# Performance work log

Hardware: AMD Instinct MI355X
Metric: run time of the kernel (lower is better)

## Reference

```python
import jax, jax.numpy as jnp
import numpy as np

N, E, C, A, R = 10000, 128000, 128, 10, 8  # nodes, edges, channels, elements, radial basis


def setup_inputs() -> dict:
    key = jax.random.key(0)
    ks = jax.random.split(key, 16)
    inp = {
        'node_attrs': jax.random.uniform(ks[0], (N, A), dtype=jnp.float32),
        'node_feats': jax.random.normal(ks[1], (N, 4 * C), dtype=jnp.float32),
        'edge_attrs': jax.random.normal(ks[2], (E, 4), dtype=jnp.float32),
        'edge_feats': jax.random.normal(ks[3], (E, R), dtype=jnp.float32),
        'edge_index': jax.random.randint(ks[4], (2, E), 0, N, dtype=jnp.int32),
        # linear_up (per-l channel mixing 128->128)
        'W_up0': jax.random.normal(ks[5], (C, C), dtype=jnp.float32),
        'W_up1': jax.random.normal(ks[6], (C, C), dtype=jnp.float32),
        # radial MLP hs=[8,64,64,64,512]
        'R0': jax.random.normal(ks[7], (R, 64), dtype=jnp.float32),
        'R1': jax.random.normal(ks[8], (64, 64), dtype=jnp.float32),
        'R2': jax.random.normal(ks[9], (64, 64), dtype=jnp.float32),
        'R3': jax.random.normal(ks[10], (64, 4 * C), dtype=jnp.float32),
        # density net hs=[8,1]
        'W_density': jax.random.normal(ks[11], (R, 1), dtype=jnp.float32),
        # linear: irreps_mid (256x0e+256x1o) -> target (128x0e+128x1o)
        'W_lin0': jax.random.normal(ks[12], (2 * C, C), dtype=jnp.float32),
        'W_lin1': jax.random.normal(ks[13], (2 * C, C), dtype=jnp.float32),
        # skip_tp: FullyConnectedTP(node_feats, node_attrs(scalars)) -> hidden
        'W_skip0': jax.random.normal(ks[14], (C, A, C), dtype=jnp.float32),
        'W_skip1': jax.random.normal(ks[15], (C, A, C), dtype=jnp.float32),
    }
    return inp


def reference(node_attrs, node_feats, edge_attrs, edge_feats, edge_index,
              W_up0, W_up1, R0, R1, R2, R3, W_density, W_lin0, W_lin1,
              W_skip0, W_skip1):
    n = node_feats.shape[0]
    silu = jax.nn.silu
    x0 = node_feats[:, :C]                       # [N,128]  l=0
    x1 = node_feats[:, C:].reshape(n, C, 3)      # [N,128,3] l=1

    # skip_tp (node_attrs are scalars -> per-element channel mixing)
    norm_skip = 1.0 / np.sqrt(C * A)
    sc0 = jnp.einsum('nu,na,uav->nv', x0, node_attrs, W_skip0) * norm_skip
    sc1 = jnp.einsum('nuk,na,uav->nvk', x1, node_attrs, W_skip1) * norm_skip
    sc = jnp.concatenate([sc0, sc1.reshape(n, 3 * C)], axis=1)  # [N,512]

    # linear_up
    h0 = (x0 @ W_up0) / np.sqrt(C)
    h1 = jnp.einsum('nuk,uv->nvk', x1, W_up1) / np.sqrt(C)

    # radial MLP -> per-edge TP weights [E, 4*C]
    w = silu((edge_feats @ R0) / np.sqrt(R))
    w = silu((w @ R1) / np.sqrt(64))
    w = silu((w @ R2) / np.sqrt(64))
    w = (w @ R3) / np.sqrt(64)
    w1, w2, w3, w4 = jnp.split(w, 4, axis=1)     # each [E,128]

    # edge density
    edge_density = jnp.tanh(((edge_feats @ W_density) / np.sqrt(R)) ** 2)  # [E,1]

    sender = edge_index[0]
    receiver = edge_index[1]
    density = jax.ops.segment_sum(edge_density, receiver, num_segments=n)  # [N,1]

    # gather sender features
    hs0 = h0[sender]   # [E,128]
    hs1 = h1[sender]   # [E,128,3]
    y0 = edge_attrs[:, :1]   # [E,1]
    y1 = edge_attrs[:, 1:4]  # [E,3]

    # uvu tensor product paths (edge_irreps x edge_attrs -> irreps_mid)
    m0a = w1 * hs0 * y0                                      # 0e x 0e -> 0e
    m0b = w4 * jnp.einsum('euk,ek->eu', hs1, y1) / np.sqrt(3.0)  # 1o x 1o -> 0e
    m1a = (w2 * hs0)[:, :, None] * y1[:, None, :]            # 0e x 1o -> 1o
    m1b = w3[:, :, None] * hs1 * y0[:, :, None]              # 1o x 0e -> 1o

    mid0 = jnp.concatenate([m0a, m0b], axis=1)               # [E,256]
    mid1 = jnp.concatenate([m1a, m1b], axis=1)               # [E,256,3]

    # scatter messages to receivers
    M0 = jax.ops.segment_sum(mid0, receiver, num_segments=n)                     # [N,256]
    M1 = jax.ops.segment_sum(mid1.reshape(-1, 2 * C * 3), receiver, num_segments=n).reshape(n, 2 * C, 3)

    # linear irreps_mid -> target, then density normalization
    denom = density + 1.0
    out0 = (M0 @ W_lin0) / np.sqrt(2 * C) / denom                               # [N,128]
    out1 = jnp.einsum('nuk,uv->nvk', M1, W_lin1) / np.sqrt(2 * C) / denom[:, :, None]

    # reshape_irreps: [N, channels, sum(2l+1)] = [N,128,4]
    message = jnp.concatenate([out0[:, :, None], out1], axis=2)
    return message, sc
```

## Files before the change

### kernel.cpp

```cpp
#include <hip/hip_runtime.h>
#include <hip/hip_bf16.h>
#include <hip/hip_fp16.h>

#define N_NODES 10000
#define N_EDGES 128000
constexpr int C = 128;
constexpr int A = 10;

constexpr float INV_SQRT_C  = 0.08838834764831845f;
constexpr float INV_SQRT_R  = 0.35355339059327373f;
constexpr float INV_SQRT_64 = 0.125f;
constexpr float INV_SQRT_CA = 0.027950849718747374f;
constexpr float INV_SQRT_2C = 0.0625f;
constexpr float INV_SQRT_3  = 0.57735026918962576f;

typedef short short8 __attribute__((ext_vector_type(8)));
typedef _Float16 f16x8 __attribute__((ext_vector_type(8)));
typedef _Float16 f16x2 __attribute__((ext_vector_type(2)));
typedef float f32x4 __attribute__((ext_vector_type(4)));

__device__ __forceinline__ float silu_f(float x) { return x / (1.0f + __expf(-x)); }

__device__ __forceinline__ void atomic_add_f32(float* p, float v) {
  __hip_atomic_fetch_add(p, v, __ATOMIC_RELAXED, __HIP_MEMORY_SCOPE_AGENT);
}

__device__ __forceinline__ unsigned short f2h(float f) {
  return __builtin_bit_cast(unsigned short, (_Float16)f);
}

__device__ __forceinline__ unsigned int pk2h(float a, float b) {
  auto h = __builtin_amdgcn_cvt_pkrtz(a, b);
  return __builtin_bit_cast(unsigned int, h);
}

__device__ __forceinline__ unsigned int pkmul_h2(unsigned int x, unsigned int y) {
  const f16x2 a = __builtin_bit_cast(f16x2, x), b = __builtin_bit_cast(f16x2, y);
  return __builtin_bit_cast(unsigned int, a * b);
}

__device__ __forceinline__ float4 h4tof4(uint2 v) {
  const __half2 lo = __builtin_bit_cast(__half2, v.x);
  const __half2 hi = __builtin_bit_cast(__half2, v.y);
  const float2 flo = __half22float2(lo), fhi = __half22float2(hi);
  return make_float4(flo.x, flo.y, fhi.x, fhi.y);
}

__global__ __launch_bounds__(256) void k_node_up(
    const float* __restrict__ nf, const float* __restrict__ Wu0,
    const float* __restrict__ Wu1, __half* __restrict__ Hh) {
  __shared__ __align__(16) float xs[8][C][4];
  const int t = threadIdx.x;
  const int n0 = blockIdx.x * 8;
  for (int idx = t; idx < 8 * 512; idx += 256) {
    const int nn = idx >> 9, q = idx & 511;
    const float val = nf[(size_t)(n0 + nn) * 512 + q];
    if (q < C) xs[nn][q][0] = val;
    else { const int r = q - C; xs[nn][r / 3][1 + r % 3] = val; }
  }
  __syncthreads();
  const int g = t >> 7, v = t & 127;
  float acc[4][4] = {};
  for (int u = 0; u < C; ++u) {
    const float w0 = Wu0[u * C + v];
    const float w1 = Wu1[u * C + v];
#pragma unroll
    for (int nn = 0; nn < 4; ++nn) {
      const float4 xv = *(const float4*)&xs[g * 4 + nn][u][0];
      acc[nn][0] = fmaf(xv.x, w0, acc[nn][0]);
      acc[nn][1] = fmaf(xv.y, w1, acc[nn][1]);
      acc[nn][2] = fmaf(xv.z, w1, acc[nn][2]);
      acc[nn][3] = fmaf(xv.w, w1, acc[nn][3]);
    }
  }
#pragma unroll
  for (int nn = 0; nn < 4; ++nn) {
    const int n = n0 + g * 4 + nn;
    uint2 o;
    o.x = pk2h(acc[nn][0] * INV_SQRT_C, acc[nn][1] * INV_SQRT_C);
    o.y = pk2h(acc[nn][2] * INV_SQRT_C, acc[nn][3] * INV_SQRT_C);
    *(uint2*)&Hh[(size_t)n * 512 + v * 4] = o;
  }
}

__device__ __forceinline__ void cvtw(const float* __restrict__ src,
                                     unsigned short* __restrict__ dst,
                                     int idx, int lgN, int KT) {
  const int k = idx >> lgN;
  const int n = idx & ((1 << lgN) - 1);
  dst[((n * KT + (k >> 5)) << 5) + (k & 31)] = f2h(src[idx]);
}

__global__ __launch_bounds__(256) void k_prep(
    const float* __restrict__ W0, const float* __restrict__ W1,
    unsigned short* __restrict__ B0, unsigned short* __restrict__ B1,
    const float* __restrict__ R1, unsigned short* __restrict__ R1a,
    const float* __restrict__ R2, unsigned short* __restrict__ R2a,
    const float* __restrict__ R3, unsigned short* __restrict__ R3a,
    const int* __restrict__ eidx, int* __restrict__ counts) {
  const int b = blockIdx.x, t = threadIdx.x;
  if (b < 640) {
    const int idx = b * 256 + t;
    const int k = idx >> 7, col = idx & 127;
    const int u = k / 10, a = k - u * 10;
    const int kp = a * 128 + u;
    const int dst = ((kp >> 5) * 128 + col) * 32 + (kp & 31);
    B0[dst] = f2h(W0[idx]);
    B1[dst] = f2h(W1[idx]);
  } else if (b < 656) {
    cvtw(R1, R1a, (b - 640) * 256 + t, 6, 2);
  } else if (b < 672) {
    cvtw(R2, R2a, (b - 656) * 256 + t, 6, 2);
  } else if (b < 800) {
    cvtw(R3, R3a, (b - 672) * 256 + t, 9, 2);
  } else {
    const int e = (b - 800) * 256 + t;
    if (e < N_EDGES) atomicAdd(&counts[eidx[N_EDGES + e]], 1);
  }
}

__global__ __launch_bounds__(256) void k_skip_mfma(
    const float* __restrict__ nf, const float* __restrict__ attrs,
    const unsigned short* __restrict__ B0, const unsigned short* __restrict__ B1,
    float* __restrict__ out_sc) {
  __shared__ __align__(16) unsigned short xs[64][136];
  __shared__ float at[64][10];
  __shared__ __align__(16) unsigned short zs[2][64][40];

  const int t = threadIdx.x;
  const int wave = t >> 6, lane = t & 63;
  const bool isG0 = blockIdx.x < 157;
  const int r0 = isG0 ? blockIdx.x * 64 : (blockIdx.x - 157) * 64;
  const int rcount = isG0 ? 10000 : 30000;
  const unsigned short* __restrict__ Bsw = isG0 ? B0 : B1;

  for (int idx = t; idx < 64 * 128; idx += 256) {
    const int i = idx >> 7, u = idx & 127;
    const int r = r0 + i;
    float v = 0.f;
    if (r < rcount) {
      if (isG0) v = nf[(size_t)r * 512 + u];
      else {
        const int n = r / 3, kc = r - n * 3;
        v = nf[(size_t)n * 512 + 128 + u * 3 + kc];
      }
    }
    xs[i][u] = f2h(v);
  }
  for (int idx = t; idx < 640; idx += 256) {
    const int i = idx / 10, a = idx - (idx / 10) * 10;
    const int r = r0 + i;
    float v = 0.f;
    if (r < rcount) v = attrs[(size_t)(isG0 ? r : r / 3) * 10 + a];
    at[i][a] = v;
  }
  __syncthreads();

  const int m = lane & 15, q = lane >> 4;
  const int colB = wave * 32;
  const int rr = t >> 2;
  const int off = (t & 3) * 8;

  unsigned int atr2[10];
#pragma unroll
  for (int a = 0; a < 10; ++a) {
    const unsigned int h = f2h(at[rr][a]);
    atr2[a] = h | (h << 16);
  }

  f32x4 acc[4][2];
#pragma unroll
  for (int rt = 0; rt < 4; ++rt)
#pragma unroll
    for (int ct = 0; ct < 2; ++ct) acc[rt][ct] = (f32x4){0.f, 0.f, 0.f, 0.f};

#pragma unroll
  for (int a = 0; a < 10; ++a) {
    const unsigned int av2 = atr2[a];
#pragma unroll
    for (int kk = 0; kk < 4; ++kk) {
      const int kt = a * 4 + kk;
      const int buf = kt & 1;
      {
        const uint4 xv = *(const uint4*)&xs[rr][kk * 32 + off];
        uint4 z;
        z.x = pkmul_h2(xv.x, av2);
        z.y = pkmul_h2(xv.y, av2);
        z.z = pkmul_h2(xv.z, av2);
        z.w = pkmul_h2(xv.w, av2);
        *(uint4*)&zs[buf][rr][off] = z;
      }
      __syncthreads();

      f16x8 bfrag[2];
#pragma unroll
      for (int ct = 0; ct < 2; ++ct) {
        const unsigned short* bp =
            &Bsw[(size_t)(kt * 128 + colB + ct * 16 + m) * 32 + q * 8];
        bfrag[ct] = *(const f16x8*)bp;
      }
#pragma unroll
      for (int rt = 0; rt < 4; ++rt) {
        const f16x8 afrag = *(const f16x8*)&zs[buf][rt * 16 + m][q * 8];
#pragma unroll
        for (int ct = 0; ct < 2; ++ct)
          acc[rt][ct] = __builtin_amdgcn_mfma_f32_16x16x32_f16(
              afrag, bfrag[ct], acc[rt][ct], 0, 0, 0);
      }
    }
  }

#pragma unroll
  for (int rt = 0; rt < 4; ++rt) {
#pragma unroll
    for (int reg = 0; reg < 4; ++reg) {
      const int rloc = rt * 16 + q * 4 + reg;
      const int r = r0 + rloc;
      if (r < rcount) {
#pragma unroll
        for (int ct = 0; ct < 2; ++ct) {
          const int v = colB + ct * 16 + m;
          const float val = acc[rt][ct][reg] * INV_SQRT_CA;
          if (isG0) {
            out_sc[(size_t)r * 512 + v] = val;
          } else {
            const int n = r / 3, kc = r - (r / 3) * 3;
            out_sc[(size_t)n * 512 + 128 + v * 3 + kc] = val;
          }
        }
      }
    }
  }
}

__global__ __launch_bounds__(1024) void k_scan(const int* __restrict__ counts,
                                               int* __restrict__ offsets,
                                               int* __restrict__ cursor) {
  __shared__ int part[1024];
  const int t = threadIdx.x;
  int local[10];
  int s = 0;
#pragma unroll
  for (int i = 0; i < 10; ++i) {
    const int idx = t * 10 + i;
    const int c = (idx < N_NODES) ? counts[idx] : 0;
    local[i] = s;
    s += c;
  }
  part[t] = s;
  __syncthreads();
  for (int off = 1; off < 1024; off <<= 1) {
    const int add = (t >= off) ? part[t - off] : 0;
    __syncthreads();
    part[t] += add;
    __syncthreads();
  }
  const int pre = (t > 0) ? part[t - 1] : 0;
#pragma unroll
  for (int i = 0; i < 10; ++i) {
    const int idx = t * 10 + i;
    if (idx < N_NODES) {
      const int o = pre + local[i];
      offsets[idx] = o;
      cursor[idx] = o;
    }
  }
  if (t == 1023) offsets[N_NODES] = part[1023];
}

__global__ __launch_bounds__(256) void k_scatter(
    const int* __restrict__ eidx, const float* __restrict__ ea_g,
    const float* __restrict__ ef_g,
    int* __restrict__ cursor,
    int* __restrict__ snd_s, int* __restrict__ rcv_s,
    float* __restrict__ ea_s, float* __restrict__ ef_s) {
  const int e = blockIdx.x * 256 + threadIdx.x;
  if (e < N_EDGES) {
    const int r = eidx[N_EDGES + e];
    const int pos = atomicAdd(&cursor[r], 1);
    snd_s[pos] = eidx[e];
    rcv_s[pos] = r;
    ((float4*)ea_s)[pos] = ((const float4*)ea_g)[e];
    ((float4*)ef_s)[pos * 2]     = ((const float4*)ef_g)[e * 2];
    ((float4*)ef_s)[pos * 2 + 1] = ((const float4*)ef_g)[e * 2 + 1];
  }
}

__global__ __launch_bounds__(256, 4) void k_mlp_msg(
    const float* __restrict__ ef_s, const float* __restrict__ ea_s,
    const int* __restrict__ snd_s, const int* __restrict__ rcv_s,
    const int* __restrict__ offsets,
    const float* __restrict__ R0, const unsigned short* __restrict__ R1a,
    const unsigned short* __restrict__ R2a, const unsigned short* __restrict__ R3a,
    const float* __restrict__ Wd, const __half* __restrict__ Hh,
    float* __restrict__ M, float* __restrict__ density) {
  __shared__ __align__(16) unsigned short actA[128][72];
  __shared__ __align__(16) unsigned char uni[18432];
  __shared__ __align__(16) float ys[128][4];
  __shared__ __align__(16) int sn[144];
  __shared__ __align__(16) int rc[128];
  float (*efs)[9] = (float (*)[9]) & uni[0];
  unsigned short (*actB)[72] = (unsigned short (*)[72]) & uni[0];
  __half (*wls2)[536] = (__half (*)[536]) & uni[0];

  const int t = threadIdx.x;
  const int wave = t >> 6, lane = t & 63, m = lane & 15, q = lane >> 4;
  const int e0 = blockIdx.x * 128;

  {
    const float4 v = *(const float4*)&ef_s[(size_t)e0 * 8 + t * 4];
    const int e = t >> 1, c0 = (t & 1) * 4;
    efs[e][c0] = v.x; efs[e][c0 + 1] = v.y;
    efs[e][c0 + 2] = v.z; efs[e][c0 + 3] = v.w;
  }
  if (t < 128) {
    *(float4*)&ys[t][0] = ((const float4*)ea_s)[e0 + t];
    sn[t] = snd_s[e0 + t];
    rc[t] = rcv_s[e0 + t];
  } else if (t < 144) {
    sn[t] = 0;
  }
  __syncthreads();

  const int u = t & 127, half = t >> 7;
  const size_t ucol = (size_t)(u << 2);
  uint2 hA[4], hB[4];
#pragma unroll
  for (int j = 0; j < 4; ++j)
    hA[j] = *(const uint2*)&Hh[(size_t)sn[j] * 512 + ucol];
#pragma unroll
  for (int j = 0; j < 4; ++j)
    hB[j] = *(const uint2*)&Hh[(size_t)sn[4 + j] * 512 + ucol];

  if (t < 128) {
    float s = 0.f;
#pragma unroll
    for (int i = 0; i < 8; ++i) s = fmaf(efs[t][i], Wd[i], s);
    s *= INV_SQRT_R;
    atomic_add_f32(&density[rc[t]], tanhf(s * s));
  }
// ... 130 lines not shown
    HX[2] = *(const uint2*)&Hh[(size_t)sn4.z * 512 + ucol];                 \
    HX[3] = *(const uint2*)&Hh[(size_t)sn4.w * 512 + ucol];                 \
  }

#pragma unroll 1
  for (int ch = 0; ch < 8; ++ch) {
    {
      const f16x8 bf0 = *(const f16x8*)&actA[ch * 16 + m][q * 8];
      const f16x8 bf1 = *(const f16x8*)&actA[ch * 16 + m][32 + q * 8];
#pragma unroll
      for (int i = 0; i < 4; ++i) {
        f32x4 cL = {0.f, 0.f, 0.f, 0.f}, cH = {0.f, 0.f, 0.f, 0.f};
        cL = __builtin_amdgcn_mfma_f32_16x16x32_f16(afL[i][0], bf0, cL, 0, 0, 0);
        cL = __builtin_amdgcn_mfma_f32_16x16x32_f16(afL[i][1], bf1, cL, 0, 0, 0);
        cH = __builtin_amdgcn_mfma_f32_16x16x32_f16(afH[i][0], bf0, cH, 0, 0, 0);
        cH = __builtin_amdgcn_mfma_f32_16x16x32_f16(afH[i][1], bf1, cH, 0, 0, 0);
        uint4 pk;
        pk.x = pk2h(cL[0] * INV_SQRT_64, cH[0] * INV_SQRT_64);
        pk.y = pk2h(cL[1] * INV_SQRT_64, cH[1] * INV_SQRT_64);
        pk.z = pk2h(cL[2] * INV_SQRT_64, cH[2] * INV_SQRT_64);
        pk.w = pk2h(cL[3] * INV_SQRT_64, cH[3] * INV_SQRT_64);
        const int JL = baseJ + i;
        const int pidx0 = ((JL < 8) ? JL * 16 : (JL - 16) * 16 + 128) + q * 4;
        *(uint4*)&wls2[m][pidx0 * 2] = pk;
      }
    }
    MSG_GROUP(0, hA)
    MSG_GROUP(1, hB)
    MSG_GROUP(2, hA)
    MSG_GROUP(3, hB)
  }
#undef MSG_GROUP
  flush(cur, s0c, s1c);
}

__global__ __launch_bounds__(256) void k_out(
    const float* __restrict__ M, const float* __restrict__ density,
    const float* __restrict__ Wl0, const float* __restrict__ Wl1,
    float* __restrict__ out) {
  __shared__ __align__(16) float Ms[8][256][4];
  __shared__ float dens[8];
  const int t = threadIdx.x;
  const int n0 = blockIdx.x * 8;
  const float4* Msrc = (const float4*)&M[(size_t)n0 * 1024];
  float4* Mdst = (float4*)&Ms[0][0][0];
  for (int idx = t; idx < 8 * 256; idx += 256) Mdst[idx] = Msrc[idx];
  if (t < 8) dens[t] = density[n0 + t] + 1.0f;
  __syncthreads();
  const int g = t >> 7, v = t & 127;
  float acc[4][4] = {};
  for (int p0 = 0; p0 < 256; p0 += 4) {
    float4 mv[4][4];
#pragma unroll
    for (int nn = 0; nn < 4; ++nn)
#pragma unroll
      for (int j = 0; j < 4; ++j)
        mv[nn][j] = *(const float4*)&Ms[g * 4 + nn][p0 + j][0];
#pragma unroll
    for (int j = 0; j < 4; ++j) {
      const float w0 = Wl0[(p0 + j) * C + v];
      const float w1 = Wl1[(p0 + j) * C + v];
#pragma unroll
      for (int nn = 0; nn < 4; ++nn) {
        acc[nn][0] = fmaf(mv[nn][j].x, w0, acc[nn][0]);
        acc[nn][1] = fmaf(mv[nn][j].y, w1, acc[nn][1]);
        acc[nn][2] = fmaf(mv[nn][j].z, w1, acc[nn][2]);
// ... 22 lines not shown
  const int*   edge_index = (const int*)d_in[4];
  const float* W_up0 = (const float*)d_in[5];
  const float* W_up1 = (const float*)d_in[6];
  const float* R0 = (const float*)d_in[7];
  const float* R1 = (const float*)d_in[8];
  const float* R2 = (const float*)d_in[9];
  const float* R3 = (const float*)d_in[10];
  const float* Wd  = (const float*)d_in[11];
  const float* Wl0 = (const float*)d_in[12];
  const float* Wl1 = (const float*)d_in[13];
  const float* Ws0 = (const float*)d_in[14];
  const float* Ws1 = (const float*)d_in[15];
  float* out = (float*)d_out;

  __half* Hh = (__half*)d_ws;
  float* M = (float*)d_ws + (size_t)N_NODES * 512;
  float* density = M + (size_t)N_NODES * 1024;
  int* counts  = (int*)(density + 10000);
  int* offsets = counts + 10016;
  int* cursor  = offsets + 10016;
  int* snd_s   = cursor + 10016;
  int* rcv_s   = snd_s + N_EDGES;
  float* ea_s  = (float*)(rcv_s + N_EDGES);
  unsigned short* Bsw0 = (unsigned short*)(ea_s + (size_t)N_EDGES * 4);
  unsigned short* Bsw1 = Bsw0 + 1280 * 128;
  unsigned short* R1a  = Bsw1 + 1280 * 128;
  unsigned short* R2a  = R1a + 64 * 64;
  unsigned short* R3a  = R2a + 64 * 64;
  float* ef_s  = (float*)(R3a + 64 * 512);

  hipMemsetAsync(M, 0, ((size_t)N_NODES * 1024 + 10000 + 10016) * sizeof(float),
                 stream);

  k_node_up<<<N_NODES / 8, 256, 0, stream>>>(node_feats, W_up0, W_up1, Hh);
  k_prep<<<1300, 256, 0, stream>>>(Ws0, Ws1, Bsw0, Bsw1, R1, R1a, R2, R2a, R3,
                                   R3a, edge_index, counts);
  k_scan<<<1, 1024, 0, stream>>>(counts, offsets, cursor);
  k_scatter<<<(N_EDGES + 255) / 256, 256, 0, stream>>>(
      edge_index, edge_attrs, edge_feats, cursor, snd_s, rcv_s, ea_s, ef_s);
  k_mlp_msg<<<N_EDGES / 128, 256, 0, stream>>>(ef_s, ea_s, snd_s, rcv_s,
                                               offsets, R0, R1a, R2a, R3a, Wd,
                                               Hh, M, density);
  k_out<<<N_NODES / 8, 256, 0, stream>>>(M, density, Wl0, Wl1, out);
  k_skip_mfma<<<157 + 469, 256, 0, stream>>>(node_feats, node_attrs, Bsw0, Bsw1,
                                             out + (size_t)N_NODES * 512);
}
```

Baseline: 329.8 us.

## Merge node-up into prep kernel and interleave skip TP blocks with message blocks

Merges the node linear_up kernel into the weight-prep/count kernel as one launch, and folds the skip tensor-product MFMA kernel into the edge MLP/message kernel. In the fused kernel, blocks alternate 8 message blocks and 5 skip blocks per group, all drawing on one shared-memory buffer. The aim is to cut launch count and tail idle time, and to overlap the compute-bound skip GEMM with the atomic-heavy message kernel. In exchange, the skip blocks now use the larger shared allocation and the launch-bounds occupancy limit of the message kernel, and the two workloads compete for the same CUs.

```diff
diff --git a/kernel.cpp b/kernel.cpp
--- a/kernel.cpp
+++ b/kernel.cpp
@@ -46,43 +46,6 @@
   return make_float4(flo.x, flo.y, fhi.x, fhi.y);
 }
 
-__global__ __launch_bounds__(256) void k_node_up(
-    const float* __restrict__ nf, const float* __restrict__ Wu0,
-    const float* __restrict__ Wu1, __half* __restrict__ Hh) {
-  __shared__ __align__(16) float xs[8][C][4];
-  const int t = threadIdx.x;
-  const int n0 = blockIdx.x * 8;
-  for (int idx = t; idx < 8 * 512; idx += 256) {
-    const int nn = idx >> 9, q = idx & 511;
-    const float val = nf[(size_t)(n0 + nn) * 512 + q];
-    if (q < C) xs[nn][q][0] = val;
-    else { const int r = q - C; xs[nn][r / 3][1 + r % 3] = val; }
-  }
-  __syncthreads();
-  const int g = t >> 7, v = t & 127;
-  float acc[4][4] = {};
-  for (int u = 0; u < C; ++u) {
-    const float w0 = Wu0[u * C + v];
-    const float w1 = Wu1[u * C + v];
-#pragma unroll
-    for (int nn = 0; nn < 4; ++nn) {
-      const float4 xv = *(const float4*)&xs[g * 4 + nn][u][0];
-      acc[nn][0] = fmaf(xv.x, w0, acc[nn][0]);
-      acc[nn][1] = fmaf(xv.y, w1, acc[nn][1]);
-      acc[nn][2] = fmaf(xv.z, w1, acc[nn][2]);
-      acc[nn][3] = fmaf(xv.w, w1, acc[nn][3]);
-    }
-  }
-#pragma unroll
-  for (int nn = 0; nn < 4; ++nn) {
-    const int n = n0 + g * 4 + nn;
-    uint2 o;
-    o.x = pk2h(acc[nn][0] * INV_SQRT_C, acc[nn][1] * INV_SQRT_C);
-    o.y = pk2h(acc[nn][2] * INV_SQRT_C, acc[nn][3] * INV_SQRT_C);
-    *(uint2*)&Hh[(size_t)n * 512 + v * 4] = o;
-  }
-}
-
 __device__ __forceinline__ void cvtw(const float* __restrict__ src,
                                      unsigned short* __restrict__ dst,
                                      int idx, int lgN, int KT) {
@@ -91,144 +54,67 @@
   dst[((n * KT + (k >> 5)) << 5) + (k & 31)] = f2h(src[idx]);
 }
 
-__global__ __launch_bounds__(256) void k_prep(
+__global__ __launch_bounds__(256) void k_prep_node(
+    const float* __restrict__ nf, const float* __restrict__ Wu0,
+    const float* __restrict__ Wu1, __half* __restrict__ Hh,
     const float* __restrict__ W0, const float* __restrict__ W1,
     unsigned short* __restrict__ B0, unsigned short* __restrict__ B1,
     const float* __restrict__ R1, unsigned short* __restrict__ R1a,
     const float* __restrict__ R2, unsigned short* __restrict__ R2a,
     const float* __restrict__ R3, unsigned short* __restrict__ R3a,
     const int* __restrict__ eidx, int* __restrict__ counts) {
-  const int b = blockIdx.x, t = threadIdx.x;
-  if (b < 640) {
-    const int idx = b * 256 + t;
-    const int k = idx >> 7, col = idx & 127;
-    const int u = k / 10, a = k - u * 10;
-    const int kp = a * 128 + u;
-    const int dst = ((kp >> 5) * 128 + col) * 32 + (kp & 31);
-    B0[dst] = f2h(W0[idx]);
-    B1[dst] = f2h(W1[idx]);
-  } else if (b < 656) {
-    cvtw(R1, R1a, (b - 640) * 256 + t, 6, 2);
-  } else if (b < 672) {
-    cvtw(R2, R2a, (b - 656) * 256 + t, 6, 2);
-  } else if (b < 800) {
-    cvtw(R3, R3a, (b - 672) * 256 + t, 9, 2);
+  __shared__ __align__(16) float xs[8][C][4];
+  const int bid = blockIdx.x, t = threadIdx.x;
+  if (bid < 1250) {
+    const int n0 = bid * 8;
+    for (int idx = t; idx < 8 * 512; idx += 256) {
+      const int nn = idx >> 9, q = idx & 511;
+      const float val = nf[(size_t)(n0 + nn) * 512 + q];
+      if (q < C) xs[nn][q][0] = val;
+      else { const int r = q - C; xs[nn][r / 3][1 + r % 3] = val; }
+    }
+    __syncthreads();
+    const int g = t >> 7, v = t & 127;
+    float acc[4][4] = {};
+    for (int u = 0; u < C; ++u) {
+      const float w0 = Wu0[u * C + v];
+      const float w1 = Wu1[u * C + v];
+#pragma unroll
+      for (int nn = 0; nn < 4; ++nn) {
+        const float4 xv = *(const float4*)&xs[g * 4 + nn][u][0];
+        acc[nn][0] = fmaf(xv.x, w0, acc[nn][0]);
+        acc[nn][1] = fmaf(xv.y, w1, acc[nn][1]);
+        acc[nn][2] = fmaf(xv.z, w1, acc[nn][2]);
+        acc[nn][3] = fmaf(xv.w, w1, acc[nn][3]);
+      }
+    }
+#pragma unroll
+    for (int nn = 0; nn < 4; ++nn) {
+      const int n = n0 + g * 4 + nn;
+      uint2 o;
+      o.x = pk2h(acc[nn][0] * INV_SQRT_C, acc[nn][1] * INV_SQRT_C);
+      o.y = pk2h(acc[nn][2] * INV_SQRT_C, acc[nn][3] * INV_SQRT_C);
+      *(uint2*)&Hh[(size_t)n * 512 + v * 4] = o;
+    }
   } else {
-    const int e = (b - 800) * 256 + t;
-    if (e < N_EDGES) atomicAdd(&counts[eidx[N_EDGES + e]], 1);
-  }
-}
-
-__global__ __launch_bounds__(256) void k_skip_mfma(
-    const float* __restrict__ nf, const float* __restrict__ attrs,
-    const unsigned short* __restrict__ B0, const unsigned short* __restrict__ B1,
-    float* __restrict__ out_sc) {
-  __shared__ __align__(16) unsigned short xs[64][136];
-  __shared__ float at[64][10];
-  __shared__ __align__(16) unsigned short zs[2][64][40];
-
-  const int t = threadIdx.x;
-  const int wave = t >> 6, lane = t & 63;
-  const bool isG0 = blockIdx.x < 157;
-  const int r0 = isG0 ? blockIdx.x * 64 : (blockIdx.x - 157) * 64;
-  const int rcount = isG0 ? 10000 : 30000;
-  const unsigned short* __restrict__ Bsw = isG0 ? B0 : B1;
-
-  for (int idx = t; idx < 64 * 128; idx += 256) {
-    const int i = idx >> 7, u = idx & 127;
-    const int r = r0 + i;
-    float v = 0.f;
-    if (r < rcount) {
-      if (isG0) v = nf[(size_t)r * 512 + u];
-      else {
-        const int n = r / 3, kc = r - n * 3;
-        v = nf[(size_t)n * 512 + 128 + u * 3 + kc];
-      }
-    }
-    xs[i][u] = f2h(v);
-  }
-  for (int idx = t; idx < 640; idx += 256) {
-    const int i = idx / 10, a = idx - (idx / 10) * 10;
-    const int r = r0 + i;
-    float v = 0.f;
-    if (r < rcount) v = attrs[(size_t)(isG0 ? r : r / 3) * 10 + a];
-    at[i][a] = v;
-  }
-  __syncthreads();
-
-  const int m = lane & 15, q = lane >> 4;
-  const int colB = wave * 32;
-  const int rr = t >> 2;
-  const int off = (t & 3) * 8;
-
-  unsigned int atr2[10];
-#pragma unroll
-  for (int a = 0; a < 10; ++a) {
-    const unsigned int h = f2h(at[rr][a]);
-    atr2[a] = h | (h << 16);
-  }
-
-  f32x4 acc[4][2];
-#pragma unroll
-  for (int rt = 0; rt < 4; ++rt)
-#pragma unroll
-    for (int ct = 0; ct < 2; ++ct) acc[rt][ct] = (f32x4){0.f, 0.f, 0.f, 0.f};
-
-#pragma unroll
-  for (int a = 0; a < 10; ++a) {
-    const unsigned int av2 = atr2[a];
-#pragma unroll
-    for (int kk = 0; kk < 4; ++kk) {
-      const int kt = a * 4 + kk;
-      const int buf = kt & 1;
-      {
-        const uint4 xv = *(const uint4*)&xs[rr][kk * 32 + off];
-        uint4 z;
-        z.x = pkmul_h2(xv.x, av2);
-        z.y = pkmul_h2(xv.y, av2);
-        z.z = pkmul_h2(xv.z, av2);
-        z.w = pkmul_h2(xv.w, av2);
-        *(uint4*)&zs[buf][rr][off] = z;
-      }
-      __syncthreads();
-
-      f16x8 bfrag[2];
-#pragma unroll
-      for (int ct = 0; ct < 2; ++ct) {
-        const unsigned short* bp =
-            &Bsw[(size_t)(kt * 128 + colB + ct * 16 + m) * 32 + q * 8];
-        bfrag[ct] = *(const f16x8*)bp;
-      }
-#pragma unroll
-      for (int rt = 0; rt < 4; ++rt) {
-        const f16x8 afrag = *(const f16x8*)&zs[buf][rt * 16 + m][q * 8];
-#pragma unroll
-        for (int ct = 0; ct < 2; ++ct)
-          acc[rt][ct] = __builtin_amdgcn_mfma_f32_16x16x32_f16(
-              afrag, bfrag[ct], acc[rt][ct], 0, 0, 0);
-      }
-    }
-  }
-
-#pragma unroll
-  for (int rt = 0; rt < 4; ++rt) {
-#pragma unroll
-    for (int reg = 0; reg < 4; ++reg) {
-      const int rloc = rt * 16 + q * 4 + reg;
-      const int r = r0 + rloc;
-      if (r < rcount) {
-#pragma unroll
-        for (int ct = 0; ct < 2; ++ct) {
-          const int v = colB + ct * 16 + m;
-          const float val = acc[rt][ct][reg] * INV_SQRT_CA;
-          if (isG0) {
-            out_sc[(size_t)r * 512 + v] = val;
-          } else {
-            const int n = r / 3, kc = r - (r / 3) * 3;
-            out_sc[(size_t)n * 512 + 128 + v * 3 + kc] = val;
-          }
-        }
-      }
+    const int b = bid - 1250;
+    if (b < 640) {
+      const int idx = b * 256 + t;
+      const int k = idx >> 7, col = idx & 127;
+      const int u = k / 10, a = k - u * 10;
+      const int kp = a * 128 + u;
+      const int dst = ((kp >> 5) * 128 + col) * 32 + (kp & 31);
+      B0[dst] = f2h(W0[idx]);
+      B1[dst] = f2h(W1[idx]);
+    } else if (b < 656) {
+      cvtw(R1, R1a, (b - 640) * 256 + t, 6, 2);
+    } else if (b < 672) {
+      cvtw(R2, R2a, (b - 656) * 256 + t, 6, 2);
+    } else if (b < 800) {
+      cvtw(R3, R3a, (b - 672) * 256 + t, 9, 2);
+    } else {
+      const int e = (b - 800) * 256 + t;
+      if (e < N_EDGES) atomicAdd(&counts[eidx[N_EDGES + e]], 1);
     }
   }
 }
@@ -286,7 +172,8 @@
   }
 }
 
-__global__ __launch_bounds__(256, 4) void k_mlp_msg(
+__device__ __forceinline__ void mlp_body(
+    int mb, unsigned char* smem,
     const float* __restrict__ ef_s, const float* __restrict__ ea_s,
     const int* __restrict__ snd_s, const int* __restrict__ rcv_s,
     const int* __restrict__ offsets,
@@ -294,18 +181,18 @@
     const unsigned short* __restrict__ R2a, const unsigned short* __restrict__ R3a,
     const float* __restrict__ Wd, const __half* __restrict__ Hh,
     float* __restrict__ M, float* __restrict__ density) {
-  __shared__ __align__(16) unsigned short actA[128][72];
-  __shared__ __align__(16) unsigned char uni[18432];
-  __shared__ __align__(16) float ys[128][4];
-  __shared__ __align__(16) int sn[144];
-  __shared__ __align__(16) int rc[128];
-  float (*efs)[9] = (float (*)[9]) & uni[0];
-  unsigned short (*actB)[72] = (unsigned short (*)[72]) & uni[0];
-  __half (*wls2)[536] = (__half (*)[536]) & uni[0];
+  unsigned short (*actA)[72] = (unsigned short (*)[72])smem;
+  unsigned char* uni = smem + 18432;
+  float (*ys)[4] = (float (*)[4])(smem + 36864);
+  int* sn = (int*)(smem + 38912);
+  int* rc = (int*)(smem + 39488);
+  float (*efs)[9] = (float (*)[9])uni;
+  unsigned short (*actB)[72] = (unsigned short (*)[72])uni;
+  __half (*wls2)[536] = (__half (*)[536])uni;
 
   const int t = threadIdx.x;
   const int wave = t >> 6, lane = t & 63, m = lane & 15, q = lane >> 4;
-  const int e0 = blockIdx.x * 128;
+  const int e0 = mb * 128;
 
   {
     const float4 v = *(const float4*)&ef_s[(size_t)e0 * 8 + t * 4];
@@ -502,6 +389,148 @@
   }
 #undef MSG_GROUP
   flush(cur, s0c, s1c);
+}
+
+__device__ __forceinline__ void skip_body(
+    int sb, unsigned char* smem,
+    const float* __restrict__ nf, const float* __restrict__ attrs,
+    const unsigned short* __restrict__ B0, const unsigned short* __restrict__ B1,
+    float* __restrict__ out_sc) {
+  unsigned short (*xs)[136] = (unsigned short (*)[136])smem;
+  float (*at)[10] = (float (*)[10])(smem + 17408);
+  unsigned short (*zs)[64][40] =
+      (unsigned short (*)[64][40])(smem + 19968);
+
+  const int t = threadIdx.x;
+  const int wave = t >> 6, lane = t & 63;
+  const bool isG0 = sb < 157;
+  const int r0 = isG0 ? sb * 64 : (sb - 157) * 64;
+  const int rcount = isG0 ? 10000 : 30000;
+  const unsigned short* __restrict__ Bsw = isG0 ? B0 : B1;
+
+  for (int idx = t; idx < 64 * 128; idx += 256) {
+    const int i = idx >> 7, u = idx & 127;
+    const int r = r0 + i;
+    float v = 0.f;
+    if (r < rcount) {
+      if (isG0) v = nf[(size_t)r * 512 + u];
+      else {
+        const int n = r / 3, kc = r - n * 3;
+        v = nf[(size_t)n * 512 + 128 + u * 3 + kc];
+      }
+    }
+    xs[i][u] = f2h(v);
+  }
+  for (int idx = t; idx < 640; idx += 256) {
+    const int i = idx / 10, a = idx - (idx / 10) * 10;
+    const int r = r0 + i;
+    float v = 0.f;
+    if (r < rcount) v = attrs[(size_t)(isG0 ? r : r / 3) * 10 + a];
+    at[i][a] = v;
+  }
+  __syncthreads();
+
+  const int m = lane & 15, q = lane >> 4;
+  const int colB = wave * 32;
+  const int rr = t >> 2;
+  const int off = (t & 3) * 8;
+
+  unsigned int atr2[10];
+#pragma unroll
+  for (int a = 0; a < 10; ++a) {
+    const unsigned int h = f2h(at[rr][a]);
+    atr2[a] = h | (h << 16);
+  }
+
+  f32x4 acc[4][2];
+#pragma unroll
+  for (int rt = 0; rt < 4; ++rt)
+#pragma unroll
+    for (int ct = 0; ct < 2; ++ct) acc[rt][ct] = (f32x4){0.f, 0.f, 0.f, 0.f};
+
+#pragma unroll
+  for (int a = 0; a < 10; ++a) {
+    const unsigned int av2 = atr2[a];
+#pragma unroll
+    for (int kk = 0; kk < 4; ++kk) {
+      const int kt = a * 4 + kk;
+      const int buf = kt & 1;
+      {
+        const uint4 xv = *(const uint4*)&xs[rr][kk * 32 + off];
+        uint4 z;
+        z.x = pkmul_h2(xv.x, av2);
+        z.y = pkmul_h2(xv.y, av2);
+        z.z = pkmul_h2(xv.z, av2);
+        z.w = pkmul_h2(xv.w, av2);
+        *(uint4*)&zs[buf][rr][off] = z;
+      }
+      __syncthreads();
+
+      f16x8 bfrag[2];
+#pragma unroll
+      for (int ct = 0; ct < 2; ++ct) {
+        const unsigned short* bp =
+            &Bsw[(size_t)(kt * 128 + colB + ct * 16 + m) * 32 + q * 8];
+        bfrag[ct] = *(const f16x8*)bp;
+      }
+#pragma unroll
+      for (int rt = 0; rt < 4; ++rt) {
+        const f16x8 afrag = *(const f16x8*)&zs[buf][rt * 16 + m][q * 8];
+#pragma unroll
+        for (int ct = 0; ct < 2; ++ct)
+          acc[rt][ct] = __builtin_amdgcn_mfma_f32_16x16x32_f16(
+              afrag, bfrag[ct], acc[rt][ct], 0, 0, 0);
+      }
+    }
+  }
+
+#pragma unroll
+  for (int rt = 0; rt < 4; ++rt) {
+#pragma unroll
+    for (int reg = 0; reg < 4; ++reg) {
+      const int rloc = rt * 16 + q * 4 + reg;
+      const int r = r0 + rloc;
+      if (r < rcount) {
+#pragma unroll
+        for (int ct = 0; ct < 2; ++ct) {
+          const int v = colB + ct * 16 + m;
+          const float val = acc[rt][ct][reg] * INV_SQRT_CA;
+          if (isG0) {
+            out_sc[(size_t)r * 512 + v] = val;
+          } else {
+            const int n = r / 3, kc = r - (r / 3) * 3;
+            out_sc[(size_t)n * 512 + 128 + v * 3 + kc] = val;
+          }
+        }
+      }
+    }
+  }
+}
+
+__global__ __launch_bounds__(256, 4) void k_fused(
+    const float* __restrict__ ef_s, const float* __restrict__ ea_s,
+    const int* __restrict__ snd_s, const int* __restrict__ rcv_s,
+    const int* __restrict__ offsets,
+    const float* __restrict__ R0, const unsigned short* __restrict__ R1a,
+    const unsigned short* __restrict__ R2a, const unsigned short* __restrict__ R3a,
+    const float* __restrict__ Wd, const __half* __restrict__ Hh,
+    float* __restrict__ M, float* __restrict__ density,
+    const float* __restrict__ nf, const float* __restrict__ attrs,
+    const unsigned short* __restrict__ B0, const unsigned short* __restrict__ B1,
+    float* __restrict__ out_sc) {
+  __shared__ __align__(16) unsigned char smem[40448];
+  const int bid = blockIdx.x;
+  if (bid < 1625) {
+    const int g = bid / 13, r = bid - g * 13;
+    if (r < 8) {
+      mlp_body(g * 8 + r, smem, ef_s, ea_s, snd_s, rcv_s, offsets, R0, R1a,
+               R2a, R3a, Wd, Hh, M, density);
+    } else {
+      skip_body(g * 5 + (r - 8), smem, nf, attrs, B0, B1, out_sc);
+    }
+  } else {
+    skip_body(625, smem, nf, attrs, B0, B1, out_sc);
+  }
 }
 
 __global__ __launch_bounds__(256) void k_out(
@@ -590,16 +619,15 @@
   hipMemsetAsync(M, 0, ((size_t)N_NODES * 1024 + 10000 + 10016) * sizeof(float),
                  stream);
 
-  k_node_up<<<N_NODES / 8, 256, 0, stream>>>(node_feats, W_up0, W_up1, Hh);
-  k_prep<<<1300, 256, 0, stream>>>(Ws0, Ws1, Bsw0, Bsw1, R1, R1a, R2, R2a, R3,
-                                   R3a, edge_index, counts);
+  k_prep_node<<<2550, 256, 0, stream>>>(node_feats, W_up0, W_up1, Hh, Ws0, Ws1,
+                                        Bsw0, Bsw1, R1, R1a, R2, R2a, R3, R3a,
+                                        edge_index, counts);
   k_scan<<<1, 1024, 0, stream>>>(counts, offsets, cursor);
   k_scatter<<<(N_EDGES + 255) / 256, 256, 0, stream>>>(
       edge_index, edge_attrs, edge_feats, cursor, snd_s, rcv_s, ea_s, ef_s);
-  k_mlp_msg<<<N_EDGES / 128, 256, 0, stream>>>(ef_s, ea_s, snd_s, rcv_s,
-                                               offsets, R0, R1a, R2a, R3a, Wd,
-                                               Hh, M, density);
+  k_fused<<<1626, 256, 0, stream>>>(ef_s, ea_s, snd_s, rcv_s, offsets, R0, R1a,
+                                    R2a, R3a, Wd, Hh, M, density, node_feats,
+                                    node_attrs, Bsw0, Bsw1,
+                                    out + (size_t)N_NODES * 512);
   k_out<<<N_NODES / 8, 256, 0, stream>>>(M, density, Wl0, Wl1, out);
-  k_skip_mfma<<<157 + 469, 256, 0, stream>>>(node_feats, node_attrs, Bsw0, Bsw1,
-                                             out + (size_t)N_NODES * 512);
-}
+}
```

Result: no change. 335.5 us (+1.7%).

## Merge node_up into prep kernel and make skip A-tile staging per-wave without barriers

Applied to the files above, without the earlier changes.

Merges the node linear-up kernel into the weight-prep/count kernel as extra blocks, removing one launch and letting the two independent pieces of work overlap. In the skip MFMA kernel, every wave now builds its own copy of the attribute-scaled A tile in a private XOR-swizzled LDS buffer, so the per-k-step __syncthreads is gone. The cost is four times the LDS writes and multiplies for the Z tile, plus a larger LDS footprint. The fused kernel also reserves the node-up shared-memory array for the prep blocks, which may lower occupancy there.

```diff
diff --git a/kernel.cpp b/kernel.cpp
--- a/kernel.cpp
+++ b/kernel.cpp
@@ -46,43 +46,6 @@
   return make_float4(flo.x, flo.y, fhi.x, fhi.y);
 }
 
-__global__ __launch_bounds__(256) void k_node_up(
-    const float* __restrict__ nf, const float* __restrict__ Wu0,
-    const float* __restrict__ Wu1, __half* __restrict__ Hh) {
-  __shared__ __align__(16) float xs[8][C][4];
-  const int t = threadIdx.x;
-  const int n0 = blockIdx.x * 8;
-  for (int idx = t; idx < 8 * 512; idx += 256) {
-    const int nn = idx >> 9, q = idx & 511;
-    const float val = nf[(size_t)(n0 + nn) * 512 + q];
-    if (q < C) xs[nn][q][0] = val;
-    else { const int r = q - C; xs[nn][r / 3][1 + r % 3] = val; }
-  }
-  __syncthreads();
-  const int g = t >> 7, v = t & 127;
-  float acc[4][4] = {};
-  for (int u = 0; u < C; ++u) {
-    const float w0 = Wu0[u * C + v];
-    const float w1 = Wu1[u * C + v];
-#pragma unroll
-    for (int nn = 0; nn < 4; ++nn) {
-      const float4 xv = *(const float4*)&xs[g * 4 + nn][u][0];
-      acc[nn][0] = fmaf(xv.x, w0, acc[nn][0]);
-      acc[nn][1] = fmaf(xv.y, w1, acc[nn][1]);
-      acc[nn][2] = fmaf(xv.z, w1, acc[nn][2]);
-      acc[nn][3] = fmaf(xv.w, w1, acc[nn][3]);
-    }
-  }
-#pragma unroll
-  for (int nn = 0; nn < 4; ++nn) {
-    const int n = n0 + g * 4 + nn;
-    uint2 o;
-    o.x = pk2h(acc[nn][0] * INV_SQRT_C, acc[nn][1] * INV_SQRT_C);
-    o.y = pk2h(acc[nn][2] * INV_SQRT_C, acc[nn][3] * INV_SQRT_C);
-    *(uint2*)&Hh[(size_t)n * 512 + v * 4] = o;
-  }
-}
-
 __device__ __forceinline__ void cvtw(const float* __restrict__ src,
                                      unsigned short* __restrict__ dst,
                                      int idx, int lgN, int KT) {
@@ -91,31 +54,68 @@
   dst[((n * KT + (k >> 5)) << 5) + (k & 31)] = f2h(src[idx]);
 }
 
-__global__ __launch_bounds__(256) void k_prep(
+__global__ __launch_bounds__(256) void k_prep_node(
+    const float* __restrict__ nf, const float* __restrict__ Wu0,
+    const float* __restrict__ Wu1, __half* __restrict__ Hh,
     const float* __restrict__ W0, const float* __restrict__ W1,
     unsigned short* __restrict__ B0, unsigned short* __restrict__ B1,
     const float* __restrict__ R1, unsigned short* __restrict__ R1a,
     const float* __restrict__ R2, unsigned short* __restrict__ R2a,
     const float* __restrict__ R3, unsigned short* __restrict__ R3a,
     const int* __restrict__ eidx, int* __restrict__ counts) {
-  const int b = blockIdx.x, t = threadIdx.x;
-  if (b < 640) {
-    const int idx = b * 256 + t;
-    const int k = idx >> 7, col = idx & 127;
-    const int u = k / 10, a = k - u * 10;
-    const int kp = a * 128 + u;
-    const int dst = ((kp >> 5) * 128 + col) * 32 + (kp & 31);
-    B0[dst] = f2h(W0[idx]);
-    B1[dst] = f2h(W1[idx]);
-  } else if (b < 656) {
-    cvtw(R1, R1a, (b - 640) * 256 + t, 6, 2);
-  } else if (b < 672) {
-    cvtw(R2, R2a, (b - 656) * 256 + t, 6, 2);
-  } else if (b < 800) {
-    cvtw(R3, R3a, (b - 672) * 256 + t, 9, 2);
+  __shared__ __align__(16) float xs[8][C][4];
+  const int bid = blockIdx.x, t = threadIdx.x;
+  if (bid < 1250) {
+    const int n0 = bid * 8;
+    for (int idx = t; idx < 8 * 512; idx += 256) {
+      const int nn = idx >> 9, q = idx & 511;
+      const float val = nf[(size_t)(n0 + nn) * 512 + q];
+      if (q < C) xs[nn][q][0] = val;
+      else { const int r = q - C; xs[nn][r / 3][1 + r % 3] = val; }
+    }
+    __syncthreads();
+    const int g = t >> 7, v = t & 127;
+    float acc[4][4] = {};
+    for (int u = 0; u < C; ++u) {
+      const float w0 = Wu0[u * C + v];
+      const float w1 = Wu1[u * C + v];
+#pragma unroll
+      for (int nn = 0; nn < 4; ++nn) {
+        const float4 xv = *(const float4*)&xs[g * 4 + nn][u][0];
+        acc[nn][0] = fmaf(xv.x, w0, acc[nn][0]);
+        acc[nn][1] = fmaf(xv.y, w1, acc[nn][1]);
+        acc[nn][2] = fmaf(xv.z, w1, acc[nn][2]);
+        acc[nn][3] = fmaf(xv.w, w1, acc[nn][3]);
+      }
+    }
+#pragma unroll
+    for (int nn = 0; nn < 4; ++nn) {
+      const int n = n0 + g * 4 + nn;
+      uint2 o;
+      o.x = pk2h(acc[nn][0] * INV_SQRT_C, acc[nn][1] * INV_SQRT_C);
+      o.y = pk2h(acc[nn][2] * INV_SQRT_C, acc[nn][3] * INV_SQRT_C);
+      *(uint2*)&Hh[(size_t)n * 512 + v * 4] = o;
+    }
   } else {
-    const int e = (b - 800) * 256 + t;
-    if (e < N_EDGES) atomicAdd(&counts[eidx[N_EDGES + e]], 1);
+    const int b = bid - 1250;
+    if (b < 640) {
+      const int idx = b * 256 + t;
+      const int k = idx >> 7, col = idx & 127;
+      const int u = k / 10, a = k - u * 10;
+      const int kp = a * 128 + u;
+      const int dst = ((kp >> 5) * 128 + col) * 32 + (kp & 31);
+      B0[dst] = f2h(W0[idx]);
+      B1[dst] = f2h(W1[idx]);
+    } else if (b < 656) {
+      cvtw(R1, R1a, (b - 640) * 256 + t, 6, 2);
+    } else if (b < 672) {
+      cvtw(R2, R2a, (b - 656) * 256 + t, 6, 2);
+    } else if (b < 800) {
+      cvtw(R3, R3a, (b - 672) * 256 + t, 9, 2);
+    } else {
+      const int e = (b - 800) * 256 + t;
+      if (e < N_EDGES) atomicAdd(&counts[eidx[N_EDGES + e]], 1);
+    }
   }
 }
 
@@ -125,7 +125,7 @@
     float* __restrict__ out_sc) {
   __shared__ __align__(16) unsigned short xs[64][136];
   __shared__ float at[64][10];
-  __shared__ __align__(16) unsigned short zs[2][64][40];
+  __shared__ __align__(16) unsigned short zsw[4][64][48];
 
   const int t = threadIdx.x;
   const int wave = t >> 6, lane = t & 63;
@@ -158,13 +158,14 @@
 
   const int m = lane & 15, q = lane >> 4;
   const int colB = wave * 32;
-  const int rr = t >> 2;
-  const int off = (t & 3) * 8;
+  unsigned short (*zw)[48] = zsw[wave];
+  const int wr_key = ((lane >> 2) & 3) << 3;
+  const int rd_key = ((m >> 2) & 3) << 3;
 
   unsigned int atr2[10];
 #pragma unroll
   for (int a = 0; a < 10; ++a) {
-    const unsigned int h = f2h(at[rr][a]);
+    const unsigned int h = f2h(at[lane][a]);
     atr2[a] = h | (h << 16);
   }
 
@@ -180,18 +181,6 @@
 #pragma unroll
     for (int kk = 0; kk < 4; ++kk) {
       const int kt = a * 4 + kk;
-      const int buf = kt & 1;
-      {
-        const uint4 xv = *(const uint4*)&xs[rr][kk * 32 + off];
-        uint4 z;
-        z.x = pkmul_h2(xv.x, av2);
-        z.y = pkmul_h2(xv.y, av2);
-        z.z = pkmul_h2(xv.z, av2);
-        z.w = pkmul_h2(xv.w, av2);
-        *(uint4*)&zs[buf][rr][off] = z;
-      }
-      __syncthreads();
-
       f16x8 bfrag[2];
 #pragma unroll
       for (int ct = 0; ct < 2; ++ct) {
@@ -199,9 +188,29 @@
             &Bsw[(size_t)(kt * 128 + colB + ct * 16 + m) * 32 + q * 8];
         bfrag[ct] = *(const f16x8*)bp;
       }
+      {
+        const uint4 xv0 = *(const uint4*)&xs[lane][kk * 32];
+        const uint4 xv1 = *(const uint4*)&xs[lane][kk * 32 + 8];
+        const uint4 xv2 = *(const uint4*)&xs[lane][kk * 32 + 16];
+        const uint4 xv3 = *(const uint4*)&xs[lane][kk * 32 + 24];
+        uint4 z;
+        z.x = pkmul_h2(xv0.x, av2); z.y = pkmul_h2(xv0.y, av2);
+        z.z = pkmul_h2(xv0.z, av2); z.w = pkmul_h2(xv0.w, av2);
+        *(uint4*)&zw[lane][0 ^ wr_key] = z;
+        z.x = pkmul_h2(xv1.x, av2); z.y = pkmul_h2(xv1.y, av2);
+        z.z = pkmul_h2(xv1.z, av2); z.w = pkmul_h2(xv1.w, av2);
+        *(uint4*)&zw[lane][8 ^ wr_key] = z;
+        z.x = pkmul_h2(xv2.x, av2); z.y = pkmul_h2(xv2.y, av2);
+        z.z = pkmul_h2(xv2.z, av2); z.w = pkmul_h2(xv2.w, av2);
+        *(uint4*)&zw[lane][16 ^ wr_key] = z;
+        z.x = pkmul_h2(xv3.x, av2); z.y = pkmul_h2(xv3.y, av2);
+        z.z = pkmul_h2(xv3.z, av2); z.w = pkmul_h2(xv3.w, av2);
+        *(uint4*)&zw[lane][24 ^ wr_key] = z;
+      }
 #pragma unroll
       for (int rt = 0; rt < 4; ++rt) {
-        const f16x8 afrag = *(const f16x8*)&zs[buf][rt * 16 + m][q * 8];
+        const f16x8 afrag =
+            *(const f16x8*)&zw[rt * 16 + m][(q * 8) ^ rd_key];
 #pragma unroll
         for (int ct = 0; ct < 2; ++ct)
           acc[rt][ct] = __builtin_amdgcn_mfma_f32_16x16x32_f16(
@@ -590,9 +599,9 @@
   hipMemsetAsync(M, 0, ((size_t)N_NODES * 1024 + 10000 + 10016) * sizeof(float),
                  stream);
 
-  k_node_up<<<N_NODES / 8, 256, 0, stream>>>(node_feats, W_up0, W_up1, Hh);
-  k_prep<<<1300, 256, 0, stream>>>(Ws0, Ws1, Bsw0, Bsw1, R1, R1a, R2, R2a, R3,
-                                   R3a, edge_index, counts);
+  k_prep_node<<<2550, 256, 0, stream>>>(node_feats, W_up0, W_up1, Hh, Ws0, Ws1,
+                                        Bsw0, Bsw1, R1, R1a, R2, R2a, R3, R3a,
+                                        edge_index, counts);
   k_scan<<<1, 1024, 0, stream>>>(counts, offsets, cursor);
   k_scatter<<<(N_EDGES + 255) / 256, 256, 0, stream>>>(
       edge_index, edge_attrs, edge_feats, cursor, snd_s, rcv_s, ea_s, ef_s);
```

New measurement: 391.3 us. 1.19x slower.

## Merge node_up into prep kernel and double-K-step skip MFMA with B prefetch

Applied to the files above, without the earlier changes.

Folds the node_up linear into the prep kernel as extra blocks, saving one launch and letting the two independent workloads share the GPU. In the skip-connection MFMA kernel, each barrier now covers two 32-wide K steps instead of one, and the B fragments for the next step are loaded into registers ahead of use. This halves the number of __syncthreads and hides global B-load latency. The cost is more register pressure and a larger zs shared buffer, and prep blocks now reserve the node_up shared array, which may reduce their occupancy.

```diff
diff --git a/kernel.cpp b/kernel.cpp
--- a/kernel.cpp
+++ b/kernel.cpp
@@ -46,43 +46,6 @@
   return make_float4(flo.x, flo.y, fhi.x, fhi.y);
 }
 
-__global__ __launch_bounds__(256) void k_node_up(
-    const float* __restrict__ nf, const float* __restrict__ Wu0,
-    const float* __restrict__ Wu1, __half* __restrict__ Hh) {
-  __shared__ __align__(16) float xs[8][C][4];
-  const int t = threadIdx.x;
-  const int n0 = blockIdx.x * 8;
-  for (int idx = t; idx < 8 * 512; idx += 256) {
-    const int nn = idx >> 9, q = idx & 511;
-    const float val = nf[(size_t)(n0 + nn) * 512 + q];
-    if (q < C) xs[nn][q][0] = val;
-    else { const int r = q - C; xs[nn][r / 3][1 + r % 3] = val; }
-  }
-  __syncthreads();
-  const int g = t >> 7, v = t & 127;
-  float acc[4][4] = {};
-  for (int u = 0; u < C; ++u) {
-    const float w0 = Wu0[u * C + v];
-    const float w1 = Wu1[u * C + v];
-#pragma unroll
-    for (int nn = 0; nn < 4; ++nn) {
-      const float4 xv = *(const float4*)&xs[g * 4 + nn][u][0];
-      acc[nn][0] = fmaf(xv.x, w0, acc[nn][0]);
-      acc[nn][1] = fmaf(xv.y, w1, acc[nn][1]);
-      acc[nn][2] = fmaf(xv.z, w1, acc[nn][2]);
-      acc[nn][3] = fmaf(xv.w, w1, acc[nn][3]);
-    }
-  }
-#pragma unroll
-  for (int nn = 0; nn < 4; ++nn) {
-    const int n = n0 + g * 4 + nn;
-    uint2 o;
-    o.x = pk2h(acc[nn][0] * INV_SQRT_C, acc[nn][1] * INV_SQRT_C);
-    o.y = pk2h(acc[nn][2] * INV_SQRT_C, acc[nn][3] * INV_SQRT_C);
-    *(uint2*)&Hh[(size_t)n * 512 + v * 4] = o;
-  }
-}
-
 __device__ __forceinline__ void cvtw(const float* __restrict__ src,
                                      unsigned short* __restrict__ dst,
                                      int idx, int lgN, int KT) {
@@ -91,31 +54,68 @@
   dst[((n * KT + (k >> 5)) << 5) + (k & 31)] = f2h(src[idx]);
 }
 
-__global__ __launch_bounds__(256) void k_prep(
+__global__ __launch_bounds__(256) void k_prep_node(
+    const float* __restrict__ nf, const float* __restrict__ Wu0,
+    const float* __restrict__ Wu1, __half* __restrict__ Hh,
     const float* __restrict__ W0, const float* __restrict__ W1,
     unsigned short* __restrict__ B0, unsigned short* __restrict__ B1,
     const float* __restrict__ R1, unsigned short* __restrict__ R1a,
     const float* __restrict__ R2, unsigned short* __restrict__ R2a,
     const float* __restrict__ R3, unsigned short* __restrict__ R3a,
     const int* __restrict__ eidx, int* __restrict__ counts) {
-  const int b = blockIdx.x, t = threadIdx.x;
-  if (b < 640) {
-    const int idx = b * 256 + t;
-    const int k = idx >> 7, col = idx & 127;
-    const int u = k / 10, a = k - u * 10;
-    const int kp = a * 128 + u;
-    const int dst = ((kp >> 5) * 128 + col) * 32 + (kp & 31);
-    B0[dst] = f2h(W0[idx]);
-    B1[dst] = f2h(W1[idx]);
-  } else if (b < 656) {
-    cvtw(R1, R1a, (b - 640) * 256 + t, 6, 2);
-  } else if (b < 672) {
-    cvtw(R2, R2a, (b - 656) * 256 + t, 6, 2);
-  } else if (b < 800) {
-    cvtw(R3, R3a, (b - 672) * 256 + t, 9, 2);
+  __shared__ __align__(16) float xs[8][C][4];
+  const int bid = blockIdx.x, t = threadIdx.x;
+  if (bid < 1250) {
+    const int n0 = bid * 8;
+    for (int idx = t; idx < 8 * 512; idx += 256) {
+      const int nn = idx >> 9, q = idx & 511;
+      const float val = nf[(size_t)(n0 + nn) * 512 + q];
+      if (q < C) xs[nn][q][0] = val;
+      else { const int r = q - C; xs[nn][r / 3][1 + r % 3] = val; }
+    }
+    __syncthreads();
+    const int g = t >> 7, v = t & 127;
+    float acc[4][4] = {};
+    for (int u = 0; u < C; ++u) {
+      const float w0 = Wu0[u * C + v];
+      const float w1 = Wu1[u * C + v];
+#pragma unroll
+      for (int nn = 0; nn < 4; ++nn) {
+        const float4 xv = *(const float4*)&xs[g * 4 + nn][u][0];
+        acc[nn][0] = fmaf(xv.x, w0, acc[nn][0]);
+        acc[nn][1] = fmaf(xv.y, w1, acc[nn][1]);
+        acc[nn][2] = fmaf(xv.z, w1, acc[nn][2]);
+        acc[nn][3] = fmaf(xv.w, w1, acc[nn][3]);
+      }
+    }
+#pragma unroll
+    for (int nn = 0; nn < 4; ++nn) {
+      const int n = n0 + g * 4 + nn;
+      uint2 o;
+      o.x = pk2h(acc[nn][0] * INV_SQRT_C, acc[nn][1] * INV_SQRT_C);
+      o.y = pk2h(acc[nn][2] * INV_SQRT_C, acc[nn][3] * INV_SQRT_C);
+      *(uint2*)&Hh[(size_t)n * 512 + v * 4] = o;
+    }
   } else {
-    const int e = (b - 800) * 256 + t;
-    if (e < N_EDGES) atomicAdd(&counts[eidx[N_EDGES + e]], 1);
+    const int b = bid - 1250;
+    if (b < 640) {
+      const int idx = b * 256 + t;
+      const int k = idx >> 7, col = idx & 127;
+      const int u = k / 10, a = k - u * 10;
+      const int kp = a * 128 + u;
+      const int dst = ((kp >> 5) * 128 + col) * 32 + (kp & 31);
+      B0[dst] = f2h(W0[idx]);
+      B1[dst] = f2h(W1[idx]);
+    } else if (b < 656) {
+      cvtw(R1, R1a, (b - 640) * 256 + t, 6, 2);
+    } else if (b < 672) {
+      cvtw(R2, R2a, (b - 656) * 256 + t, 6, 2);
+    } else if (b < 800) {
+      cvtw(R3, R3a, (b - 672) * 256 + t, 9, 2);
+    } else {
+      const int e = (b - 800) * 256 + t;
+      if (e < N_EDGES) atomicAdd(&counts[eidx[N_EDGES + e]], 1);
+    }
   }
 }
 
@@ -125,7 +125,7 @@
     float* __restrict__ out_sc) {
   __shared__ __align__(16) unsigned short xs[64][136];
   __shared__ float at[64][10];
-  __shared__ __align__(16) unsigned short zs[2][64][40];
+  __shared__ __align__(16) unsigned short zs[2][2][64][40];
 
   const int t = threadIdx.x;
   const int wave = t >> 6, lane = t & 63;
@@ -174,39 +174,56 @@
 #pragma unroll
     for (int ct = 0; ct < 2; ++ct) acc[rt][ct] = (f32x4){0.f, 0.f, 0.f, 0.f};
 
+  f16x8 bf[2][2];
+#pragma unroll
+  for (int sub = 0; sub < 2; ++sub)
+#pragma unroll
+    for (int ct = 0; ct < 2; ++ct)
+      bf[sub][ct] = *(const f16x8*)&Bsw[(size_t)(sub * 128 + colB + ct * 16 + m) * 32 + q * 8];
+
 #pragma unroll
   for (int a = 0; a < 10; ++a) {
     const unsigned int av2 = atr2[a];
 #pragma unroll
-    for (int kk = 0; kk < 4; ++kk) {
-      const int kt = a * 4 + kk;
-      const int buf = kt & 1;
-      {
+    for (int pp = 0; pp < 2; ++pp) {
+      const int p = a * 2 + pp;
+      const int buf = p & 1;
+#pragma unroll
+      for (int sub = 0; sub < 2; ++sub) {
+        const int kk = 2 * pp + sub;
         const uint4 xv = *(const uint4*)&xs[rr][kk * 32 + off];
         uint4 z;
         z.x = pkmul_h2(xv.x, av2);
         z.y = pkmul_h2(xv.y, av2);
         z.z = pkmul_h2(xv.z, av2);
         z.w = pkmul_h2(xv.w, av2);
-        *(uint4*)&zs[buf][rr][off] = z;
+        *(uint4*)&zs[buf][sub][rr][off] = z;
       }
       __syncthreads();
 
-      f16x8 bfrag[2];
-#pragma unroll
-      for (int ct = 0; ct < 2; ++ct) {
-        const unsigned short* bp =
-            &Bsw[(size_t)(kt * 128 + colB + ct * 16 + m) * 32 + q * 8];
-        bfrag[ct] = *(const f16x8*)bp;
-      }
-#pragma unroll
-      for (int rt = 0; rt < 4; ++rt) {
-        const f16x8 afrag = *(const f16x8*)&zs[buf][rt * 16 + m][q * 8];
-#pragma unroll
-        for (int ct = 0; ct < 2; ++ct)
-          acc[rt][ct] = __builtin_amdgcn_mfma_f32_16x16x32_f16(
-              afrag, bfrag[ct], acc[rt][ct], 0, 0, 0);
-      }
+      f16x8 bfn[2][2];
+      if (p < 19) {
+        const int ktn = (p + 1) * 2;
+#pragma unroll
+        for (int sub = 0; sub < 2; ++sub)
+#pragma unroll
+          for (int ct = 0; ct < 2; ++ct)
+            bfn[sub][ct] = *(const f16x8*)&Bsw[(size_t)((ktn + sub) * 128 + colB + ct * 16 + m) * 32 + q * 8];
+      }
+
+#pragma unroll
+      for (int sub = 0; sub < 2; ++sub) {
+#pragma unroll
+        for (int rt = 0; rt < 4; ++rt) {
+          const f16x8 afrag = *(const f16x8*)&zs[buf][sub][rt * 16 + m][q * 8];
+#pragma unroll
+          for (int ct = 0; ct < 2; ++ct)
+            acc[rt][ct] = __builtin_amdgcn_mfma_f32_16x16x32_f16(
+                afrag, bf[sub][ct], acc[rt][ct], 0, 0, 0);
+        }
+      }
+      bf[0][0] = bfn[0][0]; bf[0][1] = bfn[0][1];
+      bf[1][0] = bfn[1][0]; bf[1][1] = bfn[1][1];
     }
   }
 
@@ -590,9 +607,9 @@
   hipMemsetAsync(M, 0, ((size_t)N_NODES * 1024 + 10000 + 10016) * sizeof(float),
                  stream);
 
-  k_node_up<<<N_NODES / 8, 256, 0, stream>>>(node_feats, W_up0, W_up1, Hh);
-  k_prep<<<1300, 256, 0, stream>>>(Ws0, Ws1, Bsw0, Bsw1, R1, R1a, R2, R2a, R3,
-                                   R3a, edge_index, counts);
+  k_prep_node<<<2550, 256, 0, stream>>>(node_feats, W_up0, W_up1, Hh, Ws0, Ws1,
+                                        Bsw0, Bsw1, R1, R1a, R2, R2a, R3, R3a,
+                                        edge_index, counts);
   k_scan<<<1, 1024, 0, stream>>>(counts, offsets, cursor);
   k_scatter<<<(N_EDGES + 255) / 256, 256, 0, stream>>>(
       edge_index, edge_attrs, edge_feats, cursor, snd_s, rcv_s, ea_s, ef_s);
```

Result: faster. 318.9 us (-3.3%).
